# Kernel tuning notes

Measured on AMD Instinct MI355X. Metric: run time of the kernel, lower is better.

The kernel has to match this reference:

```python
import jax, jax.numpy as jnp
import numpy as np

EPS = 1e-6

D_MODEL = 1024
D_STATE = 16
D_CONV = 4
BATCH = 2
SEQ = 2048
D_INNER = 2 * D_MODEL
DT_RANK = D_MODEL // 16
D_FF = 4 * D_MODEL


def rmsnorm(x, w):
    return x * w * jax.lax.rsqrt(jnp.mean(x * x, axis=-1, keepdims=True) + EPS)


def setup_inputs() -> dict:
    key = jax.random.key(0)
    ks = jax.random.split(key, 12)
    s = lambda k, shape, scale=0.02: (jax.random.normal(k, shape, jnp.float32) * scale)
    # S4D-real style A init: A_log[d, n] = log(n+1)
    A_log = jnp.log(jnp.broadcast_to(jnp.arange(1, D_STATE + 1, dtype=jnp.float32), (D_INNER, D_STATE)))
    return {
        "x": jax.random.normal(ks[0], (BATCH, SEQ, D_MODEL), jnp.float32),
        "norm1_w": jnp.ones((D_MODEL,), jnp.float32),
        "norm2_w": jnp.ones((D_MODEL,), jnp.float32),
        "in_proj_w": s(ks[1], (2 * D_INNER, D_MODEL)),
        "conv_w": s(ks[2], (D_INNER, 1, D_CONV), 0.2),
        "conv_b": jnp.zeros((D_INNER,), jnp.float32),
        "x_proj_w": s(ks[3], (DT_RANK + 2 * D_STATE, D_INNER)),
        "dt_proj_w": s(ks[4], (D_INNER, DT_RANK), 0.1),
        "dt_proj_b": jax.random.uniform(ks[5], (D_INNER,), jnp.float32, -4.0, -3.0),
        "A_log": A_log,
        "D": jnp.ones((D_INNER,), jnp.float32),
        "out_proj_w": s(ks[6], (D_MODEL, D_INNER)),
        "w1": s(ks[7], (D_FF, D_MODEL)),
        "w3": s(ks[8], (D_FF, D_MODEL)),
        "w2": s(ks[9], (D_MODEL, D_FF)),
    }


def _ssm(h, in_proj_w, conv_w, conv_b, x_proj_w, dt_proj_w, dt_proj_b, A_log, D, out_proj_w):
    d_inner, d_state = A_log.shape
    dt_rank = dt_proj_w.shape[1]
    d_conv = conv_w.shape[-1]
    bsz = h.shape[0]

    xz = jnp.einsum('bld,ed->ble', h, in_proj_w)          # (B, L, 2*d_inner)
    xin, z = jnp.split(xz, 2, axis=-1)

    # causal depthwise conv over time
    xc = jnp.swapaxes(xin, 1, 2)                           # (B, d_inner, L)
    xc = jax.lax.conv_general_dilated(xc, conv_w, (1,), [(d_conv - 1, 0)],
                                      feature_group_count=d_inner)
    xin = jax.nn.silu(jnp.swapaxes(xc + conv_b[:, None], 1, 2))  # (B, L, d_inner)

    x_dbl = jnp.einsum('bld,ed->ble', xin, x_proj_w)       # (B, L, dt_rank + 2*d_state)
    dt, Bm, Cm = jnp.split(x_dbl, [dt_rank, dt_rank + d_state], axis=-1)
    delta = jax.nn.softplus(jnp.einsum('blr,dr->bld', dt, dt_proj_w) + dt_proj_b)
    A = -jnp.exp(A_log)                                    # (d_inner, d_state)

    def step(hstate, t):
        delta_t, B_t, C_t, x_t = t                         # (B,d), (B,n), (B,n), (B,d)
        dA = jnp.exp(delta_t[..., None] * A)               # (B, d_inner, d_state)
        dBx = (delta_t * x_t)[..., None] * B_t[:, None, :]
        hstate = dA * hstate + dBx
        y = jnp.einsum('bdn,bn->bd', hstate, C_t)
        return hstate, y

    tm = lambda a: jnp.swapaxes(a, 0, 1)                   # time-major
    h0 = jnp.zeros((bsz, d_inner, d_state), h.dtype)
    _, ys = jax.lax.scan(step, h0, (tm(delta), tm(Bm), tm(Cm), tm(xin)))
    y = jnp.swapaxes(ys, 0, 1) + xin * D                   # (B, L, d_inner)
    return jnp.einsum('bld,ed->ble', y * jax.nn.silu(z), out_proj_w)


def reference(x, norm1_w, norm2_w, in_proj_w, conv_w, conv_b, x_proj_w,
              dt_proj_w, dt_proj_b, A_log, D, out_proj_w, w1, w3, w2):
    x = x + _ssm(rmsnorm(x, norm1_w), in_proj_w, conv_w, conv_b, x_proj_w,
                 dt_proj_w, dt_proj_b, A_log, D, out_proj_w)
    h = rmsnorm(x, norm2_w)
    mlp = jnp.einsum('blf,df->bld',
                     jax.nn.silu(jnp.einsum('bld,fd->blf', h, w1)) * jnp.einsum('bld,fd->blf', h, w3),
                     w2)
    return x + mlp
```

## Files before the change

### kernel.cpp

```cpp
#include <hip/hip_runtime.h>

#define DEV __device__ __forceinline__

typedef unsigned short u16;
typedef float f32x4 __attribute__((ext_vector_type(4)));
typedef __bf16 bf16x8 __attribute__((ext_vector_type(8)));

#define CHUNK 64
#define NCH 32

DEV u16 f2b(float f) {
    unsigned u = __builtin_bit_cast(unsigned, f);
    u += 0x7fffu + ((u >> 16) & 1u);
    return (u16)(u >> 16);
}
DEV float b2f(u16 h) { return __builtin_bit_cast(float, (unsigned)h << 16); }
DEV float silu_(float v) { return v / (1.f + __expf(-v)); }
DEV float b2f_lo(unsigned w) { return __builtin_bit_cast(float, w << 16); }
DEV float b2f_hi(unsigned w) { return __builtin_bit_cast(float, w & 0xffff0000u); }
DEV void unpack8(uint4 w, float* f) {
    f[0] = b2f_lo(w.x); f[1] = b2f_hi(w.x);
    f[2] = b2f_lo(w.y); f[3] = b2f_hi(w.y);
    f[4] = b2f_lo(w.z); f[5] = b2f_hi(w.z);
    f[6] = b2f_lo(w.w); f[7] = b2f_hi(w.w);
}

DEV void gload16(const void* g, void* l) {
    __builtin_amdgcn_global_load_lds((const __attribute__((address_space(1))) unsigned int*)g,
                                     (__attribute__((address_space(3))) unsigned int*)l,
                                     16, 0, 0);
}

__global__ __launch_bounds__(256) void cvt_bf16_k(const float* __restrict__ in,
                                                  u16* __restrict__ out, int n4) {
    int i = blockIdx.x * 256 + threadIdx.x;
    if (i >= n4) return;
    float4 v = reinterpret_cast<const float4*>(in)[i];
    ushort4 o;
    o.x = f2b(v.x); o.y = f2b(v.y); o.z = f2b(v.z); o.w = f2b(v.w);
    reinterpret_cast<ushort4*>(out)[i] = o;
}

__global__ __launch_bounds__(256) void addred_k(const float* __restrict__ resid,
                                                const u16* __restrict__ p0,
                                                const u16* __restrict__ p1,
                                                float* __restrict__ out, int n4) {
    int i = blockIdx.x * 256 + threadIdx.x;
    if (i >= n4) return;
    float4 rv = reinterpret_cast<const float4*>(resid)[i];
    ushort4 a = reinterpret_cast<const ushort4*>(p0)[i];
    ushort4 b = reinterpret_cast<const ushort4*>(p1)[i];
    float4 o;
    o.x = rv.x + b2f(a.x) + b2f(b.x);
    o.y = rv.y + b2f(a.y) + b2f(b.y);
    o.z = rv.z + b2f(a.z) + b2f(b.z);
    o.w = rv.w + b2f(a.w) + b2f(b.w);
    reinterpret_cast<float4*>(out)[i] = o;
}

__global__ __launch_bounds__(256) void rmsnorm_k(const float* __restrict__ x,
                                                 const float* __restrict__ w,
                                                 u16* __restrict__ out) {
    int row = blockIdx.x;
    int t = threadIdx.x;
    float4 v = reinterpret_cast<const float4*>(x + (size_t)row * 1024)[t];
    float s = v.x * v.x + v.y * v.y + v.z * v.z + v.w * v.w;
#pragma unroll
    for (int off = 32; off; off >>= 1) s += __shfl_xor(s, off);
    __shared__ float red[4];
    if ((t & 63) == 0) red[t >> 6] = s;
    __syncthreads();
    float tot = red[0] + red[1] + red[2] + red[3];
    float scale = rsqrtf(tot * (1.f / 1024.f) + 1e-6f);
    float4 wv = reinterpret_cast<const float4*>(w)[t];
    ushort4 o;
    o.x = f2b(v.x * wv.x * scale);
    o.y = f2b(v.y * wv.y * scale);
    o.z = f2b(v.z * wv.z * scale);
    o.w = f2b(v.w * wv.w * scale);
    reinterpret_cast<ushort4*>(out + (size_t)row * 1024)[t] = o;
}

template <int EPI, bool SPLIT = false>
__global__ __launch_bounds__(256) void gemm_bt(
    const u16* __restrict__ A, int lda,
    const u16* __restrict__ B, int ldb,
    void* C, int ldc,
    int N, int K,
    const float* __restrict__ bias,
    const void* aux, int ldaux) {
    __shared__ u16 lsA[128 * 32];
    __shared__ u16 lsB[128 * 32];
    const int t = threadIdx.x;
    const int l = t & 63, w = t >> 6;

    int nwg = gridDim.x * gridDim.y;
    int bid = blockIdx.y * gridDim.x + blockIdx.x;
    int cpx = nwg >> 3;
    int swz = (bid & 7) * cpx + (bid >> 3);
    const int m0 = (swz % gridDim.x) * 128, n0 = (swz / gridDim.x) * 128;

    int klo = 0, klen = K;
    if constexpr (SPLIT) { klen = K >> 1; klo = blockIdx.z * klen; }

    const int wm = w >> 1, wn = w & 1;
    const int lrow = l & 15, lk8 = (l >> 4) * 8;

    const int sr = w * 16 + (l >> 2);
    const int sc = (l & 3) * 8;
    const u16* gA0 = A + (size_t)(m0 + sr) * lda + sc + klo;
    const u16* gA1 = gA0 + (size_t)64 * lda;
    int nr0 = n0 + sr;      if (nr0 > N - 1) nr0 = N - 1;
    int nr1 = n0 + 64 + sr; if (nr1 > N - 1) nr1 = N - 1;
    const u16* gB0 = B + (size_t)nr0 * ldb + sc + klo;
    const u16* gB1 = B + (size_t)nr1 * ldb + sc + klo;
    u16* ldsA0 = &lsA[w * 512];
    u16* ldsA1 = &lsA[2048 + w * 512];
    u16* ldsB0 = &lsB[w * 512];
    u16* ldsB1 = &lsB[2048 + w * 512];

    f32x4 acc[4][4];
#pragma unroll
    for (int i = 0; i < 4; ++i)
#pragma unroll
        for (int j = 0; j < 4; ++j) acc[i][j] = (f32x4){0.f, 0.f, 0.f, 0.f};

    for (int k0 = 0; k0 < klen; k0 += 32) {
        gload16(gA0 + k0, ldsA0);
        gload16(gA1 + k0, ldsA1);
        gload16(gB0 + k0, ldsB0);
        gload16(gB1 + k0, ldsB1);
        __syncthreads();
        bf16x8 af[4], bfr[4];
#pragma unroll
        for (int i = 0; i < 4; ++i)
            af[i] = *reinterpret_cast<const bf16x8*>(&lsA[(wm * 64 + i * 16 + lrow) * 32 + lk8]);
#pragma unroll
        for (int j = 0; j < 4; ++j)
            bfr[j] = *reinterpret_cast<const bf16x8*>(&lsB[(wn * 64 + j * 16 + lrow) * 32 + lk8]);
#pragma unroll
        for (int i = 0; i < 4; ++i)
#pragma unroll
            for (int j = 0; j < 4; ++j)
                acc[i][j] = __builtin_amdgcn_mfma_f32_16x16x32_bf16(af[i], bfr[j], acc[i][j], 0, 0, 0);
        __syncthreads();
    }

    u16* Cp = (u16*)C;
    if constexpr (SPLIT)
        Cp += (size_t)blockIdx.z * gridDim.x * 128 * ldc;

    const int rbase = m0 + wm * 64 + (l >> 4) * 4;
    const int cbase = n0 + wn * 64 + (l & 15);
#pragma unroll
    for (int i = 0; i < 4; ++i) {
#pragma unroll
        for (int j = 0; j < 4; ++j) {
            int col = cbase + j * 16;
            if (col >= N) continue;
#pragma unroll
            for (int r = 0; r < 4; ++r) {
                int row = rbase + i * 16 + r;
                float v = acc[i][j][r];
                size_t idx = (size_t)row * ldc + col;
                if constexpr (EPI == 0) {
                    Cp[idx] = f2b(v);
                } else if constexpr (EPI == 1) {
                    float z = v + bias[col];
                    float sp = z > 20.f ? z : log1pf(__expf(z));
                    Cp[idx] = f2b(sp);
                } else if constexpr (EPI == 2) {
                    ((float*)C)[idx] = v + ((const float*)aux)[(size_t)row * ldaux + col];
                } else if constexpr (EPI == 4) {
                    float g = b2f(((const u16*)aux)[(size_t)row * ldaux + col]);
                    Cp[idx] = f2b(silu_(g) * v);
                } else if constexpr (EPI == 5) {
                    if (col < 2048)
                        ((u16*)C)[(size_t)row * ldc + col] = f2b(v);
                    else
                        ((u16*)aux)[(size_t)row * ldaux + (col - 2048)] = f2b(v);
                }
            }
        }
    }
}

__global__ __launch_bounds__(256) void conv_k(const u16* __restrict__ xraw,
                                              const float* __restrict__ cw,
                                              const float* __restrict__ cb,
                                              u16* __restrict__ xin) {
    size_t idx = (size_t)blockIdx.x * 256 + threadIdx.x;
    if (idx >= (size_t)4096 * 2048) return;
    int d = (int)(idx & 2047);
    int m = (int)(idx >> 11);
    int lpos = m & 2047, b = m >> 11;
    float acc = cb[d];
#pragma unroll
    for (int j = 0; j < 4; ++j) {
        int lj = lpos - 3 + j;
        if (lj >= 0)
            acc += b2f(xraw[((size_t)(b * 2048 + lj) << 11) + d]) * cw[d * 4 + j];
    }
    xin[idx] = f2b(silu_(acc));
}

__global__ __launch_bounds__(256) void scan_p1(const u16* __restrict__ dlt,
                                               const u16* __restrict__ xin,
                                               const u16* __restrict__ xdbl,
                                               const float* __restrict__ A_log,
                                               float* __restrict__ hfin,
                                               float* __restrict__ sdlt) {
    int blk = blockIdx.x;
    int g = blk & 7, c = (blk >> 3) & 31, b = blk >> 8;
    int d = g * 256 + threadIdx.x;
    __shared__ u16 bc[CHUNK * 32];
    {
        int i = threadIdx.x;
        int r = i >> 2, q = i & 3;
        const u16* src = xdbl + ((size_t)(b * 2048 + c * CHUNK + r) * 96 + 64 + q * 8);
        *reinterpret_cast<uint4*>(&bc[r * 32 + q * 8]) = *reinterpret_cast<const uint4*>(src);
    }
    __syncthreads();
    float A2[16];
#pragma unroll
    for (int n = 0; n < 16; ++n) A2[n] = -__expf(A_log[d * 16 + n]) * 1.44269504f;
    float h[16];
#pragma unroll
    for (int n = 0; n < 16; ++n) h[n] = 0.f;
    float S = 0.f;
    size_t base = ((size_t)(b * 2048 + c * CHUNK) << 11) + d;
#pragma unroll 4
    for (int t = 0; t < CHUNK; ++t) {
        float dl = b2f(dlt[base + ((size_t)t << 11)]);
        float xv = b2f(xin[base + ((size_t)t << 11)]);
        S += dl;
        float dx = dl * xv;
        float Bv[16];
        unpack8(*reinterpret_cast<const uint4*>(&bc[t * 32]), Bv);
        unpack8(*reinterpret_cast<const uint4*>(&bc[t * 32 + 8]), Bv + 8);
#pragma unroll
        for (int n = 0; n < 16; ++n)
            h[n] = __builtin_amdgcn_exp2f(dl * A2[n]) * h[n] + dx * Bv[n];
    }
    float* hf = hfin + ((size_t)((b * NCH + c) * 2048 + d) << 4);
#pragma unroll
    for (int n = 0; n < 4; ++n)
        reinterpret_cast<float4*>(hf)[n] = (float4){h[4*n], h[4*n+1], h[4*n+2], h[4*n+3]};
    sdlt[(b * NCH + c) * 2048 + d] = S;
}

__global__ __launch_bounds__(256) void scan_p2(const float* __restrict__ hfin,
                                               const float* __restrict__ sdlt,
                                               const float* __restrict__ A_log,
                                               float* __restrict__ hini) {
    int t = blockIdx.x * 256 + threadIdx.x;
    int n = t & 15, d = (t >> 4) & 2047, b = t >> 15;
    float A2 = -__expf(A_log[d * 16 + n]) * 1.44269504f;
    float h = 0.f;
    for (int c = 0; c < NCH; ++c) {
        size_t idx = ((size_t)((b * NCH + c) * 2048 + d) << 4) + n;
        hini[idx] = h;
        float P = __builtin_amdgcn_exp2f(A2 * sdlt[(b * NCH + c) * 2048 + d]);
        h = P * h + hfin[idx];
    }
}

__global__ __launch_bounds__(256) void scan_p3(const u16* __restrict__ dlt,
                                               const u16* __restrict__ xin,
                                               const u16* __restrict__ xdbl,
                                               const u16* __restrict__ zb,
                                               const float* __restrict__ A_log,
                                               const float* __restrict__ Dv,
                                               const float* __restrict__ hini,
                                               u16* __restrict__ y2) {
    int blk = blockIdx.x;
    int g = blk & 7, c = (blk >> 3) & 31, b = blk >> 8;
    int d = g * 256 + threadIdx.x;
    __shared__ u16 bc[CHUNK * 32];
    {
        int i = threadIdx.x;
        int r = i >> 2, q = i & 3;
        const u16* src = xdbl + ((size_t)(b * 2048 + c * CHUNK + r) * 96 + 64 + q * 8);
        *reinterpret_cast<uint4*>(&bc[r * 32 + q * 8]) = *reinterpret_cast<const uint4*>(src);
    }
    __syncthreads();
    float A2[16];
#pragma unroll
    for (int n = 0; n < 16; ++n) A2[n] = -__expf(A_log[d * 16 + n]) * 1.44269504f;
    float h[16];
    const float* hi = hini + ((size_t)((b * NCH + c) * 2048 + d) << 4);
#pragma unroll
    for (int n = 0; n < 4; ++n) {
        float4 v = reinterpret_cast<const float4*>(hi)[n];
        h[4*n] = v.x; h[4*n+1] = v.y; h[4*n+2] = v.z; h[4*n+3] = v.w;
    }
    float Dd = Dv[d];
    size_t base = ((size_t)(b * 2048 + c * CHUNK) << 11) + d;
#pragma unroll 4
    for (int t = 0; t < CHUNK; ++t) {
        float dl = b2f(dlt[base + ((size_t)t << 11)]);
        float xv = b2f(xin[base + ((size_t)t << 11)]);
        float zv = b2f(zb[base + ((size_t)t << 11)]);
        float dx = dl * xv;
        float Bv[16], Cv[16];
        unpack8(*reinterpret_cast<const uint4*>(&bc[t * 32]), Bv);
        unpack8(*reinterpret_cast<const uint4*>(&bc[t * 32 + 8]), Bv + 8);
        unpack8(*reinterpret_cast<const uint4*>(&bc[t * 32 + 16]), Cv);
        unpack8(*reinterpret_cast<const uint4*>(&bc[t * 32 + 24]), Cv + 8);
        float y = 0.f;
#pragma unroll
        for (int n = 0; n < 16; ++n) {
            h[n] = __builtin_amdgcn_exp2f(dl * A2[n]) * h[n] + dx * Bv[n];
            y += h[n] * Cv[n];
        }
        y = (y + xv * Dd) * silu_(zv);
        y2[base + ((size_t)t << 11)] = f2b(y);
    }
}

extern "C" void kernel_launch(void* const* d_in, const int* in_sizes, int n_in,
                              void* d_out, int out_size, void* d_ws, size_t ws_size,
                              hipStream_t stream) {
    const float* x         = (const float*)d_in[0];
    const float* n1w       = (const float*)d_in[1];
    const float* n2w       = (const float*)d_in[2];
    const float* w_inproj  = (const float*)d_in[3];
    const float* conv_w    = (const float*)d_in[4];
    const float* conv_b    = (const float*)d_in[5];
    const float* x_projw   = (const float*)d_in[6];
    const float* w_dtproj  = (const float*)d_in[7];
    const float* dt_b      = (const float*)d_in[8];
    const float* A_log     = (const float*)d_in[9];
    const float* Dv        = (const float*)d_in[10];
    const float* w_outproj = (const float*)d_in[11];
    const float* w1        = (const float*)d_in[12];
    const float* w3        = (const float*)d_in[13];
    const float* w2        = (const float*)d_in[14];

    char* ws = (char*)d_ws;
    u16* wbuf    = (u16*)(ws + 0);
    u16* h_bf    = (u16*)(ws + 8388608);
    u16* xraw_bf = (u16*)(ws + 16777216);
    u16* z_bf    = (u16*)(ws + 33554432);
    u16* xin_bf  = (u16*)(ws + 50331648);
    u16* dlt_bf  = (u16*)(ws + 67108864);
    u16* xdbl_bf = (u16*)(ws + 83886080);
    float* sdlt  = (float*)(ws + 84672512);
    float* hfin  = (float*)wbuf;
    float* hini  = (float*)h_bf;
    u16* y2_bf   = xraw_bf;
    float* x2_f  = (float*)(ws + 67108864);
    u16* g1_bf   = xraw_bf;
    u16* act_bf  = g1_bf;
    u16* pOP     = z_bf;
    u16* pW2     = xin_bf;
    const size_t PSTRIDE = (size_t)4096 * 1024;

    auto cvt = [&](const float* src, int n) {
        int n4 = n >> 2;
        cvt_bf16_k<<<(n4 + 255) / 256, 256, 0, stream>>>(src, wbuf, n4);
    };

    rmsnorm_k<<<4096, 256, 0, stream>>>(x, n1w, h_bf);
    cvt(w_inproj, 4096 * 1024);
    gemm_bt<5><<<dim3(32, 32), 256, 0, stream>>>(h_bf, 1024, wbuf, 1024, xraw_bf, 2048,
                                                 4096, 1024, nullptr, z_bf, 2048);
    conv_k<<<32768, 256, 0, stream>>>(xraw_bf, conv_w, conv_b, xin_bf);
    cvt(x_projw, 96 * 2048);
    gemm_bt<0><<<dim3(32, 1), 256, 0, stream>>>(xin_bf, 2048, wbuf, 2048, xdbl_bf, 96,
                                                96, 2048, nullptr, nullptr, 0);
    cvt(w_dtproj, 2048 * 64);
    gemm_bt<1><<<dim3(32, 16), 256, 0, stream>>>(xdbl_bf, 96, wbuf, 64, dlt_bf, 2048,
                                                 2048, 64, dt_b, nullptr, 0);
    scan_p1<<<512, 256, 0, stream>>>(dlt_bf, xin_bf, xdbl_bf, A_log, hfin, sdlt);
    scan_p2<<<256, 256, 0, stream>>>(hfin, sdlt, A_log, hini);
    scan_p3<<<512, 256, 0, stream>>>(dlt_bf, xin_bf, xdbl_bf, z_bf, A_log, Dv, hini, y2_bf);
    cvt(w_outproj, 1024 * 2048);
    gemm_bt<0, true><<<dim3(32, 8, 2), 256, 0, stream>>>(y2_bf, 2048, wbuf, 2048, pOP, 1024,
                                                         1024, 2048, nullptr, nullptr, 0);
    addred_k<<<4096, 256, 0, stream>>>(x, pOP, pOP + PSTRIDE, x2_f, 4096 * 1024 / 4);
    rmsnorm_k<<<4096, 256, 0, stream>>>(x2_f, n2w, h_bf);
    cvt(w1, 4096 * 1024);
    gemm_bt<0><<<dim3(32, 32), 256, 0, stream>>>(h_bf, 1024, wbuf, 1024, g1_bf, 4096,
                                                 4096, 1024, nullptr, nullptr, 0);
    cvt(w3, 4096 * 1024);
    gemm_bt<4><<<dim3(32, 32), 256, 0, stream>>>(h_bf, 1024, wbuf, 1024, act_bf, 4096,
                                                 4096, 1024, nullptr, g1_bf, 4096);
    cvt(w2, 1024 * 4096);
    gemm_bt<0, true><<<dim3(32, 8, 2), 256, 0, stream>>>(act_bf, 4096, wbuf, 4096, pW2, 1024,
                                                         1024, 4096, nullptr, nullptr, 0);
    addred_k<<<4096, 256, 0, stream>>>(x2_f, pW2, pW2 + PSTRIDE, (float*)d_out, 4096 * 1024 / 4);
}
```

Baseline: 705.8 us.

## Double-buffer GEMM LDS tiles and fuse w1/w3 gate GEMMs into one kernel

The GEMM main loop now double-buffers shared-memory tiles, so the global load for the next K tile is issued before the MFMAs on the current tile and one barrier per iteration is removed. A new NB=2 variant loads two B matrices, computes both w1 and w3 products against the same A tile, and applies silu(g)*v in the epilogue. This drops the separate g1 intermediate write and read and one load of the h activations. In exchange, shared memory use doubles (triples for NB=2) and the fused kernel holds twice the accumulator registers, which may reduce occupancy.

```diff
diff --git a/kernel.cpp b/kernel.cpp
--- a/kernel.cpp
+++ b/kernel.cpp
@@ -81,16 +81,18 @@
     reinterpret_cast<ushort4*>(out + (size_t)row * 1024)[t] = o;
 }
 
-template <int EPI, bool SPLIT = false>
+template <int EPI, int NB = 1, bool SPLIT = false>
 __global__ __launch_bounds__(256) void gemm_bt(
     const u16* __restrict__ A, int lda,
     const u16* __restrict__ B, int ldb,
     void* C, int ldc,
     int N, int K,
     const float* __restrict__ bias,
-    const void* aux, int ldaux) {
-    __shared__ u16 lsA[128 * 32];
-    __shared__ u16 lsB[128 * 32];
+    const void* aux, int ldaux,
+    const u16* __restrict__ B2) {
+    __shared__ u16 lsA[2 * 4096];
+    __shared__ u16 lsB[2 * 4096];
+    __shared__ u16 lsB2[NB == 2 ? 2 * 4096 : 2];
     const int t = threadIdx.x;
     const int l = t & 63, w = t >> 6;
 
@@ -114,36 +116,69 @@
     int nr1 = n0 + 64 + sr; if (nr1 > N - 1) nr1 = N - 1;
     const u16* gB0 = B + (size_t)nr0 * ldb + sc + klo;
     const u16* gB1 = B + (size_t)nr1 * ldb + sc + klo;
-    u16* ldsA0 = &lsA[w * 512];
-    u16* ldsA1 = &lsA[2048 + w * 512];
-    u16* ldsB0 = &lsB[w * 512];
-    u16* ldsB1 = &lsB[2048 + w * 512];
-
-    f32x4 acc[4][4];
-#pragma unroll
-    for (int i = 0; i < 4; ++i)
-#pragma unroll
-        for (int j = 0; j < 4; ++j) acc[i][j] = (f32x4){0.f, 0.f, 0.f, 0.f};
-
-    for (int k0 = 0; k0 < klen; k0 += 32) {
-        gload16(gA0 + k0, ldsA0);
-        gload16(gA1 + k0, ldsA1);
-        gload16(gB0 + k0, ldsB0);
-        gload16(gB1 + k0, ldsB1);
+    const u16* gB20 = nullptr;
+    const u16* gB21 = nullptr;
+    if constexpr (NB == 2) {
+        gB20 = B2 + (size_t)nr0 * ldb + sc + klo;
+        gB21 = B2 + (size_t)nr1 * ldb + sc + klo;
+    }
+
+    f32x4 acc[NB][4][4];
+#pragma unroll
+    for (int p = 0; p < NB; ++p)
+#pragma unroll
+        for (int i = 0; i < 4; ++i)
+#pragma unroll
+            for (int j = 0; j < 4; ++j) acc[p][i][j] = (f32x4){0.f, 0.f, 0.f, 0.f};
+
+    auto stage = [&](int buf, int kt) {
+        const int k0 = kt << 5;
+        const int bo = buf << 12;
+        gload16(gA0 + k0, &lsA[bo + w * 512]);
+        gload16(gA1 + k0, &lsA[bo + 2048 + w * 512]);
+        gload16(gB0 + k0, &lsB[bo + w * 512]);
+        gload16(gB1 + k0, &lsB[bo + 2048 + w * 512]);
+        if constexpr (NB == 2) {
+            gload16(gB20 + k0, &lsB2[bo + w * 512]);
+            gload16(gB21 + k0, &lsB2[bo + 2048 + w * 512]);
+        }
+    };
+
+    const int nt = klen >> 5;
+    stage(0, 0);
+    __syncthreads();
+    int cur = 0;
+    for (int kt = 0; kt < nt; ++kt) {
+        if (kt + 1 < nt) stage(cur ^ 1, kt + 1);
+        const int bo = cur << 12;
+        bf16x8 af[4], bfr[4];
+#pragma unroll
+        for (int i = 0; i < 4; ++i)
+            af[i] = *reinterpret_cast<const bf16x8*>(&lsA[bo + (wm * 64 + i * 16 + lrow) * 32 + lk8]);
+#pragma unroll
+        for (int j = 0; j < 4; ++j)
+            bfr[j] = *reinterpret_cast<const bf16x8*>(&lsB[bo + (wn * 64 + j * 16 + lrow) * 32 + lk8]);
+        if constexpr (NB == 2) {
+            bf16x8 b2r[4];
+#pragma unroll
+            for (int j = 0; j < 4; ++j)
+                b2r[j] = *reinterpret_cast<const bf16x8*>(&lsB2[bo + (wn * 64 + j * 16 + lrow) * 32 + lk8]);
+#pragma unroll
+            for (int i = 0; i < 4; ++i)
+#pragma unroll
+                for (int j = 0; j < 4; ++j) {
+                    acc[0][i][j] = __builtin_amdgcn_mfma_f32_16x16x32_bf16(af[i], bfr[j], acc[0][i][j], 0, 0, 0);
+                    acc[1][i][j] = __builtin_amdgcn_mfma_f32_16x16x32_bf16(af[i], b2r[j], acc[1][i][j], 0, 0, 0);
+                }
+        } else {
+#pragma unroll
+            for (int i = 0; i < 4; ++i)
+#pragma unroll
+                for (int j = 0; j < 4; ++j)
+                    acc[0][i][j] = __builtin_amdgcn_mfma_f32_16x16x32_bf16(af[i], bfr[j], acc[0][i][j], 0, 0, 0);
+        }
         __syncthreads();
-        bf16x8 af[4], bfr[4];
-#pragma unroll
-        for (int i = 0; i < 4; ++i)
-            af[i] = *reinterpret_cast<const bf16x8*>(&lsA[(wm * 64 + i * 16 + lrow) * 32 + lk8]);
-#pragma unroll
-        for (int j = 0; j < 4; ++j)
-            bfr[j] = *reinterpret_cast<const bf16x8*>(&lsB[(wn * 64 + j * 16 + lrow) * 32 + lk8]);
-#pragma unroll
-        for (int i = 0; i < 4; ++i)
-#pragma unroll
-            for (int j = 0; j < 4; ++j)
-                acc[i][j] = __builtin_amdgcn_mfma_f32_16x16x32_bf16(af[i], bfr[j], acc[i][j], 0, 0, 0);
-        __syncthreads();
+        cur ^= 1;
     }
 
     u16* Cp = (u16*)C;
@@ -161,7 +196,7 @@
 #pragma unroll
             for (int r = 0; r < 4; ++r) {
                 int row = rbase + i * 16 + r;
-                float v = acc[i][j][r];
+                float v = acc[0][i][j][r];
                 size_t idx = (size_t)row * ldc + col;
                 if constexpr (EPI == 0) {
                     Cp[idx] = f2b(v);
@@ -179,6 +214,8 @@
                         ((u16*)C)[(size_t)row * ldc + col] = f2b(v);
                     else
                         ((u16*)aux)[(size_t)row * ldaux + (col - 2048)] = f2b(v);
+                } else if constexpr (EPI == 6) {
+                    Cp[idx] = f2b(silu_(v) * acc[NB - 1][i][j][r]);
                 }
             }
         }
@@ -350,44 +387,42 @@
     float* hini  = (float*)h_bf;
     u16* y2_bf   = xraw_bf;
     float* x2_f  = (float*)(ws + 67108864);
-    u16* g1_bf   = xraw_bf;
-    u16* act_bf  = g1_bf;
+    u16* act_bf  = xraw_bf;
+    u16* wbuf3   = xin_bf;
     u16* pOP     = z_bf;
     u16* pW2     = xin_bf;
     const size_t PSTRIDE = (size_t)4096 * 1024;
 
-    auto cvt = [&](const float* src, int n) {
+    auto cvt = [&](const float* src, u16* dst, int n) {
         int n4 = n >> 2;
-        cvt_bf16_k<<<(n4 + 255) / 256, 256, 0, stream>>>(src, wbuf, n4);
+        cvt_bf16_k<<<(n4 + 255) / 256, 256, 0, stream>>>(src, dst, n4);
     };
 
     rmsnorm_k<<<4096, 256, 0, stream>>>(x, n1w, h_bf);
-    cvt(w_inproj, 4096 * 1024);
+    cvt(w_inproj, wbuf, 4096 * 1024);
     gemm_bt<5><<<dim3(32, 32), 256, 0, stream>>>(h_bf, 1024, wbuf, 1024, xraw_bf, 2048,
-                                                 4096, 1024, nullptr, z_bf, 2048);
+                                                 4096, 1024, nullptr, z_bf, 2048, nullptr);
     conv_k<<<32768, 256, 0, stream>>>(xraw_bf, conv_w, conv_b, xin_bf);
-    cvt(x_projw, 96 * 2048);
+    cvt(x_projw, wbuf, 96 * 2048);
     gemm_bt<0><<<dim3(32, 1), 256, 0, stream>>>(xin_bf, 2048, wbuf, 2048, xdbl_bf, 96,
-                                                96, 2048, nullptr, nullptr, 0);
-    cvt(w_dtproj, 2048 * 64);
+                                                96, 2048, nullptr, nullptr, 0, nullptr);
+    cvt(w_dtproj, wbuf, 2048 * 64);
     gemm_bt<1><<<dim3(32, 16), 256, 0, stream>>>(xdbl_bf, 96, wbuf, 64, dlt_bf, 2048,
-                                                 2048, 64, dt_b, nullptr, 0);
+                                                 2048, 64, dt_b, nullptr, 0, nullptr);
     scan_p1<<<512, 256, 0, stream>>>(dlt_bf, xin_bf, xdbl_bf, A_log, hfin, sdlt);
     scan_p2<<<256, 256, 0, stream>>>(hfin, sdlt, A_log, hini);
     scan_p3<<<512, 256, 0, stream>>>(dlt_bf, xin_bf, xdbl_bf, z_bf, A_log, Dv, hini, y2_bf);
-    cvt(w_outproj, 1024 * 2048);
-    gemm_bt<0, true><<<dim3(32, 8, 2), 256, 0, stream>>>(y2_bf, 2048, wbuf, 2048, pOP, 1024,
-                                                         1024, 2048, nullptr, nullptr, 0);
+    cvt(w_outproj, wbuf, 1024 * 2048);
+    gemm_bt<0, 1, true><<<dim3(32, 8, 2), 256, 0, stream>>>(y2_bf, 2048, wbuf, 2048, pOP, 1024,
+                                                            1024, 2048, nullptr, nullptr, 0, nullptr);
     addred_k<<<4096, 256, 0, stream>>>(x, pOP, pOP + PSTRIDE, x2_f, 4096 * 1024 / 4);
     rmsnorm_k<<<4096, 256, 0, stream>>>(x2_f, n2w, h_bf);
-    cvt(w1, 4096 * 1024);
-    gemm_bt<0><<<dim3(32, 32), 256, 0, stream>>>(h_bf, 1024, wbuf, 1024, g1_bf, 4096,
-                                                 4096, 1024, nullptr, nullptr, 0);
-    cvt(w3, 4096 * 1024);
-    gemm_bt<4><<<dim3(32, 32), 256, 0, stream>>>(h_bf, 1024, wbuf, 1024, act_bf, 4096,
-                                                 4096, 1024, nullptr, g1_bf, 4096);
-    cvt(w2, 1024 * 4096);
-    gemm_bt<0, true><<<dim3(32, 8, 2), 256, 0, stream>>>(act_bf, 4096, wbuf, 4096, pW2, 1024,
-                                                         1024, 4096, nullptr, nullptr, 0);
+    cvt(w1, wbuf, 4096 * 1024);
+    cvt(w3, wbuf3, 4096 * 1024);
+    gemm_bt<6, 2><<<dim3(32, 32), 256, 0, stream>>>(h_bf, 1024, wbuf, 1024, act_bf, 4096,
+                                                    4096, 1024, nullptr, nullptr, 0, wbuf3);
+    cvt(w2, wbuf, 1024 * 4096);
+    gemm_bt<0, 1, true><<<dim3(32, 8, 2), 256, 0, stream>>>(act_bf, 4096, wbuf, 4096, pW2, 1024,
+                                                            1024, 4096, nullptr, nullptr, 0, nullptr);
     addred_k<<<4096, 256, 0, stream>>>(x2_f, pW2, pW2 + PSTRIDE, (float*)d_out, 4096 * 1024 / 4);
 }
```

Result: no change. 702.9 us (-0.4%).
